# Kernel optimization log

Measured on AMD Instinct MI355X. Metric: run time of the kernel, lower is better.

## Reference

```python
import jax, jax.numpy as jnp
import numpy as np
import math

HIDDEN = 256
NUM_LAYERS = 3
NUM_TAU = 4
DT = 0.05
TAU_MIN, TAU_MAX = 0.01, 10.0
IN_SIZE = 128
OUT_SIZE = 64
B, S = 64, 2048


def setup_inputs() -> dict:
    key = jax.random.key(0)
    ks = jax.random.split(key, 16)
    H = HIDDEN
    def xavier(k, shape):
        fan_in, fan_out = shape[1], shape[0]
        lim = math.sqrt(6.0 / (fan_in + fan_out))
        return jax.random.uniform(k, shape, jnp.float32, -lim, lim)
    def ortho(k, n):
        a = jax.random.normal(k, (n, n), jnp.float32)
        q, r = jnp.linalg.qr(a)
        return q * jnp.sign(jnp.diag(r))[None, :]
    x = jax.random.normal(ks[0], (B, S, IN_SIZE), jnp.float32)
    # complexity_net: Linear(in,64) -> ReLU -> Linear(64,1) -> Sigmoid
    cw1 = xavier(ks[1], (64, IN_SIZE)); cb1 = jnp.zeros((64,), jnp.float32)
    cw2 = xavier(ks[2], (1, 64)); cb2 = jnp.zeros((1,), jnp.float32)
    # input projection
    pw = xavier(ks[3], (H, IN_SIZE)); pb = jnp.zeros((H,), jnp.float32)
    # per-layer recurrent params (stacked over layers)
    W_rec = jnp.stack([ortho(jax.random.fold_in(ks[4], i), H) for i in range(NUM_LAYERS)])
    W_in = jnp.stack([xavier(jax.random.fold_in(ks[5], i), (H, H)) for i in range(NUM_LAYERS)])
    bias = jnp.zeros((NUM_LAYERS, H), jnp.float32)
    tau_bands = jnp.tile(jnp.logspace(math.log10(TAU_MIN), math.log10(TAU_MAX), NUM_TAU, dtype=jnp.float32)[None, :], (NUM_LAYERS, 1))
    # tau_mixer: Linear(1, NUM_TAU) per layer -> weight [NUM_TAU,1] stored as [NUM_TAU]
    tmw = jax.random.uniform(ks[6], (NUM_LAYERS, NUM_TAU), jnp.float32, -1.0, 1.0)
    tmb = jax.random.uniform(ks[7], (NUM_LAYERS, NUM_TAU), jnp.float32, -1.0, 1.0)
    # output projection
    ow = xavier(ks[8], (OUT_SIZE, H)); ob = jnp.zeros((OUT_SIZE,), jnp.float32)
    return {"x": x, "cw1": cw1, "cb1": cb1, "cw2": cw2, "cb2": cb2,
            "pw": pw, "pb": pb, "W_rec": W_rec, "W_in": W_in, "bias": bias,
            "tau_bands": tau_bands, "tmw": tmw, "tmb": tmb, "ow": ow, "ob": ob}


def reference(x, cw1, cb1, cw2, cb2, pw, pb, W_rec, W_in, bias, tau_bands, tmw, tmb, ow, ob):
    # complexity net on time-mean of inputs -> [B, 1]
    comp = jax.nn.sigmoid(jax.nn.relu(x.mean(axis=1) @ cw1.T + cb1) @ cw2.T + cb2)
    h_seq = x @ pw.T + pb  # [B, S, H]
    hidden = jnp.zeros((x.shape[0], HIDDEN), x.dtype)
    for i in range(NUM_LAYERS):
        # tau_mixer: comp [B,1] * weight [NUM_TAU] -> logits [B, NUM_TAU]
        w = jax.nn.softmax(comp * tmw[i] + tmb[i], axis=-1)
        mixed_tau = jnp.sum(tau_bands[i] * w, axis=-1)          # [B]
        alpha = jnp.exp(-DT / mixed_tau)[:, None]               # [B,1] broadcast over H
        Wr, Wi, b = W_rec[i], W_in[i], bias[i]
        ext = h_seq @ Wi.T + b                                  # precompute input drive [B,S,H]
        def step(h, xt):
            act = jnp.tanh(h @ Wr.T + xt)
            h_new = alpha * h + (1.0 - alpha) * act
            return h_new, h_new
        hidden, outs = jax.lax.scan(step, hidden, ext.transpose(1, 0, 2))
        h_seq = outs.transpose(1, 0, 2)                         # [B,S,H]
    out = h_seq @ ow.T + ob                                     # [B,S,out]
    return out[:, -1]                                           # [B,out]
```

## Files before the change

### kernel.cpp

```cpp
#include <hip/hip_runtime.h>
#include <hip/hip_bf16.h>
#include <math.h>
#include <type_traits>

#define HIDDEN 256
#define SEQ 2048
#define BATCH 64
#define INSZ 128
#define OUTSZ 64
#define DTC 0.05f
#define CCH 32
#define CHS (SEQ / CCH)
#define TBLK (CHS / 32)

typedef _Float16 f16x8 __attribute__((ext_vector_type(8)));
typedef float f32x4 __attribute__((ext_vector_type(4)));

__global__ __launch_bounds__(1024) void prep_kernel(
    const float* __restrict__ x, const float* __restrict__ cw1, const float* __restrict__ cb1,
    const float* __restrict__ cw2, const float* __restrict__ cb2,
    const float* __restrict__ tau_b, const float* __restrict__ tmw, const float* __restrict__ tmb,
    float* __restrict__ alphas, float* __restrict__ h_carry)
{
    __shared__ float p_lds[8][128];
    __shared__ float xm[128];
    __shared__ float t1[64];
    int b = blockIdx.x;
    int tid = threadIdx.x;
    if (tid < 256) {
        h_carry[0 * 16384 + b * 256 + tid] = 0.f;
        h_carry[1 * 16384 + b * 256 + tid] = 0.f;
        h_carry[2 * 16384 + b * 256 + tid] = 0.f;
    }
    int c = tid & 127, sh = tid >> 7;
    const float* xb = x + (size_t)b * SEQ * INSZ;
    float s = 0.f;
    for (int t = sh * 256; t < (sh + 1) * 256; ++t) s += xb[(size_t)t * INSZ + c];
    p_lds[sh][c] = s;
    __syncthreads();
    if (tid < 128) {
        float m = 0.f;
        #pragma unroll
        for (int i = 0; i < 8; ++i) m += p_lds[i][tid];
        xm[tid] = m / (float)SEQ;
    }
    __syncthreads();
    if (tid < 64) {
        float acc = cb1[tid];
        for (int k = 0; k < 128; ++k) acc += xm[k] * cw1[tid * 128 + k];
        t1[tid] = fmaxf(acc, 0.f);
    }
    __syncthreads();
    if (tid == 0) {
        float acc = cb2[0];
        for (int k = 0; k < 64; ++k) acc += t1[k] * cw2[k];
        float comp = 1.f / (1.f + expf(-acc));
        for (int i = 0; i < 3; ++i) {
            float lg[4], mx = -1e30f;
            for (int j = 0; j < 4; ++j) { lg[j] = comp * tmw[i * 4 + j] + tmb[i * 4 + j]; mx = fmaxf(mx, lg[j]); }
            float den = 0.f;
            for (int j = 0; j < 4; ++j) { lg[j] = expf(lg[j] - mx); den += lg[j]; }
            float mt = 0.f;
            for (int j = 0; j < 4; ++j) mt += tau_b[i * 4 + j] * (lg[j] / den);
            alphas[i * 64 + b] = expf(-DTC / mt);
        }
    }
}

__global__ __launch_bounds__(128) void wf_kernel(
    const float* __restrict__ W_in0, const float* __restrict__ pw,
    const float* __restrict__ pb, const float* __restrict__ bias0,
    float* __restrict__ Wf, float* __restrict__ bf)
{
    __shared__ float wrow[256];
    int j = blockIdx.x, k = threadIdx.x;
    for (int m = k; m < 256; m += 128) wrow[m] = W_in0[j * 256 + m];
    __syncthreads();
    float s = 0.f;
    for (int m = 0; m < 256; ++m) s = fmaf(wrow[m], pw[m * 128 + k], s);
    Wf[j * 128 + k] = s;
    if (k == 0) {
        float sb = bias0[j];
        for (int m = 0; m < 256; ++m) sb = fmaf(wrow[m], pb[m], sb);
        bf[j] = sb;
    }
}

__device__ __forceinline__ unsigned pkrtz(float a, float b) {
    return __builtin_bit_cast(unsigned, __builtin_amdgcn_cvt_pkrtz(a, b));
}

__global__ __launch_bounds__(64) void wpack_kernel(
    const float* __restrict__ W, _Float16* __restrict__ P)
{
    int blk = blockIdx.x;
    int wave = blk >> 5, mt = (blk >> 3) & 3, kt = blk & 7;
    int lane = threadIdx.x;
    int row = wave * 64 + mt * 16 + (lane & 15);
    int kcol = kt * 32 + (lane >> 4) * 8;
    const float4* s = (const float4*)(W + (size_t)row * 256 + kcol);
    float4 a = s[0], b = s[1];
    uint4 u = { pkrtz(a.x, a.y), pkrtz(a.z, a.w), pkrtz(b.x, b.y), pkrtz(b.z, b.w) };
    *(uint4*)((char*)P + (size_t)blk * 1024 + lane * 16) = u;
}

__device__ __forceinline__ float fast_tanh(float x) {
    float ex = __expf(2.f * x);
    float r = __builtin_amdgcn_rcpf(ex + 1.f);
    return 1.f - 2.f * r;
}

__device__ __forceinline__ void barrier_lds_only() {
    asm volatile("s_waitcnt lgkmcnt(0)\n\ts_barrier" ::: "memory");
}

__global__ __launch_bounds__(256, 2) void gemm0_kernel(
    const float* __restrict__ Asrc,
    const float* __restrict__ W,
    const float* __restrict__ bias,
    float* __restrict__ C)
{
    constexpr int KD = 128, KT = 4, ROWB = 256;
    __shared__ alignas(16) char alds[32 * ROWB];
    const int tid = threadIdx.x;
    const int wave = tid >> 6, lane = tid & 63;
    const int bl = lane & 15, q = lane >> 4;
    const int m0 = blockIdx.x * 32;

    f16x8 bfrag[4][KT];
    float bv[4];
    #pragma unroll
    for (int nt = 0; nt < 4; ++nt) {
        int n = wave * 64 + nt * 16 + bl;
        const float* wr = W + (size_t)n * KD;
        #pragma unroll
        for (int kt = 0; kt < KT; ++kt) {
            const float4* wp = (const float4*)(wr + kt * 32 + q * 8);
            float4 u0 = wp[0], u1 = wp[1];
            uint4 u = { pkrtz(u0.x, u0.y), pkrtz(u0.z, u0.w),
                        pkrtz(u1.x, u1.y), pkrtz(u1.z, u1.w) };
            bfrag[nt][kt] = __builtin_bit_cast(f16x8, u);
        }
        bv[nt] = bias[n];
    }
    #pragma unroll
    for (int it = 0; it < 2; ++it) {
        int idx = tid + it * 256;
        int row = idx >> 4, chunk = idx & 15;
        const float4* sp = (const float4*)(Asrc + (size_t)(m0 + row) * KD + chunk * 8);
        float4 f0 = sp[0], f1 = sp[1];
        uint4 u = { pkrtz(f0.x, f0.y), pkrtz(f0.z, f0.w),
                    pkrtz(f1.x, f1.y), pkrtz(f1.z, f1.w) };
        *(uint4*)(alds + row * ROWB + ((chunk * 16) ^ ((row & 7) << 4))) = u;
    }
    __syncthreads();

    f32x4 acc[2][4];
    #pragma unroll
    for (int mt = 0; mt < 2; ++mt)
        #pragma unroll
        for (int nt = 0; nt < 4; ++nt) acc[mt][nt] = (f32x4){0.f, 0.f, 0.f, 0.f};
    #pragma unroll
    for (int kt = 0; kt < KT; ++kt) {
        int inner = kt * 64 + q * 16;
        f16x8 a0 = __builtin_bit_cast(f16x8,
            *(const uint4*)(alds + (0 * 16 + bl) * ROWB + (inner ^ ((bl & 7) << 4))));
        f16x8 a1 = __builtin_bit_cast(f16x8,
            *(const uint4*)(alds + (1 * 16 + bl) * ROWB + (inner ^ ((bl & 7) << 4))));
        #pragma unroll
        for (int nt = 0; nt < 4; ++nt) {
            acc[0][nt] = __builtin_amdgcn_mfma_f32_16x16x32_f16(a0, bfrag[nt][kt], acc[0][nt], 0, 0, 0);
            acc[1][nt] = __builtin_amdgcn_mfma_f32_16x16x32_f16(a1, bfrag[nt][kt], acc[1][nt], 0, 0, 0);
        }
    }
    #pragma unroll
    for (int mt = 0; mt < 2; ++mt)
        #pragma unroll
        for (int nt = 0; nt < 4; ++nt) {
            int col = wave * 64 + nt * 16 + bl;
            #pragma unroll
            for (int r = 0; r < 4; ++r)
                C[(size_t)(m0 + mt * 16 + q * 4 + r) * 256 + col] = acc[mt][nt][r] + bv[nt];
        }
}

__device__ __forceinline__ void scan_chunk(
    char* smem, float* buf, const _Float16* __restrict__ Wp,
    const float* __restrict__ alphas, float* __restrict__ h_carry,
    int b, int c, int write_all)
{
    _Float16 (*hlds)[256] = (_Float16 (*)[256])smem;
    const int tid = threadIdx.x;
    const int wave = tid >> 6, lane = tid & 63;
    const int bl = lane & 15, q = lane >> 4;
    const int mt_own = bl >> 2, r_own = bl & 3;
    const int m = wave * 64 + mt_own * 16 + q * 4 + r_own;

    f16x8 afrag[4][8];
    #pragma unroll
    for (int mt = 0; mt < 4; ++mt)
        #pragma unroll
        for (int kt = 0; kt < 8; ++kt)
            afrag[mt][kt] = __builtin_bit_cast(f16x8,
                *(const uint4*)((const char*)Wp + (size_t)(((wave * 4 + mt) * 8 + kt) * 64 + lane) * 16));

    const float alpha = alphas[b], onema = 1.f - alpha;
    float* bb = buf + (size_t)b * SEQ * HIDDEN;
    const int t0 = c * CHS, tend = t0 + CHS;

    float h_reg = h_carry[b * 256 + m];
    hlds[0][m] = (_Float16)h_reg;
    float e_cur = bb[(size_t)t0 * HIDDEN + m];
    float e_n1  = bb[(size_t)(t0 + 1) * HIDDEN + m];
    __syncthreads();

    auto step = [&](auto CB, int t) {
        constexpr int CUR = decltype(CB)::value;
        const char* rb = (const char*)&hlds[CUR][0];
        uint4 bq0 = *(const uint4*)(rb + q * 16);
        uint4 bq1 = *(const uint4*)(rb + 64 + q * 16);
        uint4 bq2 = *(const uint4*)(rb + 128 + q * 16);
        uint4 bq3 = *(const uint4*)(rb + 192 + q * 16);
        uint4 bq4 = *(const uint4*)(rb + 256 + q * 16);
        uint4 bq5 = *(const uint4*)(rb + 320 + q * 16);
        uint4 bq6 = *(const uint4*)(rb + 384 + q * 16);
        uint4 bq7 = *(const uint4*)(rb + 448 + q * 16);
        float e_n2 = 0.f;
        if (t + 2 < tend) e_n2 = bb[(size_t)(t + 2) * HIDDEN + m];

        f32x4 a0 = {0.f,0.f,0.f,0.f}, a1 = {0.f,0.f,0.f,0.f};
        f32x4 a2 = {0.f,0.f,0.f,0.f}, a3 = {0.f,0.f,0.f,0.f};
        #define MSTEP(BQ, KT) { f16x8 bf = __builtin_bit_cast(f16x8, BQ);                  \
            a0 = __builtin_amdgcn_mfma_f32_16x16x32_f16(afrag[0][KT], bf, a0, 0, 0, 0);    \
            a1 = __builtin_amdgcn_mfma_f32_16x16x32_f16(afrag[1][KT], bf, a1, 0, 0, 0);    \
            a2 = __builtin_amdgcn_mfma_f32_16x16x32_f16(afrag[2][KT], bf, a2, 0, 0, 0);    \
            a3 = __builtin_amdgcn_mfma_f32_16x16x32_f16(afrag[3][KT], bf, a3, 0, 0, 0); }
        MSTEP(bq0, 0) MSTEP(bq1, 1) MSTEP(bq2, 2) MSTEP(bq3, 3)
        MSTEP(bq4, 4) MSTEP(bq5, 5) MSTEP(bq6, 6) MSTEP(bq7, 7)
        #undef MSTEP

        f32x4 am = (mt_own == 0) ? a0 : (mt_own == 1) ? a1 : (mt_own == 2) ? a2 : a3;
        float s  = (r_own == 0) ? am[0] : (r_own == 1) ? am[1] : (r_own == 2) ? am[2] : am[3];

        float act = fast_tanh(s + e_cur);
        h_reg = alpha * h_reg + onema * act;
        hlds[CUR ^ 1][m] = (_Float16)h_reg;
        if (write_all)
            *((_Float16*)(bb + (size_t)t * HIDDEN) + m) = (_Float16)h_reg;
        barrier_lds_only();
        e_cur = e_n1;
        e_n1 = e_n2;
    };

    for (int t = t0; t < tend; t += 2) {
        step(std::integral_constant<int, 0>{}, t);
        step(std::integral_constant<int, 1>{}, t + 1);
    }
    h_carry[b * 256 + m] = h_reg;
}

__device__ __forceinline__ void gemm_chunk4(
    char* smem, float* buf, const _Float16* __restrict__ Wp,
    const float* __restrict__ bias, int gl, int c)
{
    constexpr int KT = 8, ROWB = 512;
    char* alds = smem;
    const int tid = threadIdx.x;
    const int wave = tid >> 6, lane = tid & 63;
    const int bl = lane & 15, q = lane >> 4;

    f16x8 bfrag[4][KT];
    float bv[4];
    #pragma unroll
    for (int nt = 0; nt < 4; ++nt) {
        #pragma unroll
        for (int kt = 0; kt < KT; ++kt)
            bfrag[nt][kt] = __builtin_bit_cast(f16x8,
                *(const uint4*)((const char*)Wp + (size_t)(((wave * 4 + nt) * 8 + kt) * 64 + lane) * 16));
        bv[nt] = bias[wave * 64 + nt * 16 + bl];
    }

    for (int u = 0; u < 2 * TBLK; ++u) {
        int b = 2 * gl + (u >> 1);
        int half = u & 1;
        size_t m0 = (size_t)b * SEQ + (size_t)c * CHS + (size_t)half * 32;

        __syncthreads();
        #pragma unroll
        for (int it = 0; it < 4; ++it) {
            int idx = tid + it * 256;
            int row = idx >> 5, chunk = idx & 31;
            uint4 uu = *(const uint4*)((const char*)buf + (m0 + row) * 1024 + chunk * 16);
            *(uint4*)(alds + row * ROWB + ((chunk * 16) ^ ((row & 7) << 4))) = uu;
        }
        __syncthreads();

        f32x4 acc[2][4];
        #pragma unroll
        for (int mt = 0; mt < 2; ++mt)
            #pragma unroll
            for (int nt = 0; nt < 4; ++nt) acc[mt][nt] = (f32x4){0.f, 0.f, 0.f, 0.f};
        #pragma unroll
        for (int kt = 0; kt < KT; ++kt) {
            int inner = kt * 64 + q * 16;
            f16x8 a0 = __builtin_bit_cast(f16x8,
                *(const uint4*)(alds + (0 * 16 + bl) * ROWB + (inner ^ ((bl & 7) << 4))));
            f16x8 a1 = __builtin_bit_cast(f16x8,
                *(const uint4*)(alds + (1 * 16 + bl) * ROWB + (inner ^ ((bl & 7) << 4))));
            #pragma unroll
            for (int nt = 0; nt < 4; ++nt) {
                acc[0][nt] = __builtin_amdgcn_mfma_f32_16x16x32_f16(a0, bfrag[nt][kt], acc[0][nt], 0, 0, 0);
                acc[1][nt] = __builtin_amdgcn_mfma_f32_16x16x32_f16(a1, bfrag[nt][kt], acc[1][nt], 0, 0, 0);
            }
        }
        #pragma unroll
        for (int mt = 0; mt < 2; ++mt)
            #pragma unroll
            for (int nt = 0; nt < 4; ++nt) {
                int col = wave * 64 + nt * 16 + bl;
                #pragma unroll
                for (int r = 0; r < 4; ++r)
                    buf[(m0 + mt * 16 + q * 4 + r) * 256 + col] = acc[mt][nt][r] + bv[nt];
            }
    }
}

__global__ __launch_bounds__(256, 1) void stage_kernel(
    int stage, float* buf,
    const _Float16* __restrict__ wpk,
    const float* __restrict__ bias,  const float* __restrict__ alphas,
    float* __restrict__ h_carry)
{
    __shared__ alignas(16) char smem[16384];
    int blk = blockIdx.x;
    if (blk < 192) {
        int layer = blk >> 6;
        int c = stage - 2 * layer;
        if (c < 0 || c >= CCH) return;
        scan_chunk(smem, buf, wpk + (size_t)layer * 65536, alphas + layer * 64,
                   h_carry + (size_t)layer * 16384, blk & 63, c, layer < 2);
    } else {
        int g = blk - 192;
        int which = g >> 5;
        int gl = g & 31;
        int c = stage - 1 - 2 * which;
        if (c < 0 || c >= CCH) return;
        gemm_chunk4(smem, buf, wpk + (size_t)(3 + which) * 65536, bias + (which + 1) * 256, gl, c);
    }
}

__global__ __launch_bounds__(256) void outproj_kernel(
    const float* __restrict__ h_carry, const float* __restrict__ ow, const float* __restrict__ ob,
    float* __restrict__ out)
{
    __shared__ float h_l[256];
    __shared__ float p_lds[4][64];
    int b = blockIdx.x;
    int tid = threadIdx.x;
    h_l[tid] = h_carry[b * 256 + tid];
    __syncthreads();
    int o = tid & 63, qq = tid >> 6;
    float s = 0.f;
    const float4* wp = (const float4*)(ow + o * 256 + qq * 64);
    const float4* hp = (const float4*)(h_l + qq * 64);
    #pragma unroll
    for (int m = 0; m < 16; ++m) {
        float4 wv = wp[m]; float4 hv = hp[m];
        s = fmaf(wv.x, hv.x, s); s = fmaf(wv.y, hv.y, s);
        s = fmaf(wv.z, hv.z, s); s = fmaf(wv.w, hv.w, s);
    }
    p_lds[qq][o] = s;
    __syncthreads();
    if (tid < 64)
        out[b * 64 + tid] = p_lds[0][tid] + p_lds[1][tid] + p_lds[2][tid] + p_lds[3][tid] + ob[tid];
}

extern "C" void kernel_launch(void* const* d_in, const int* in_sizes, int n_in,
                              void* d_out, int out_size, void* d_ws, size_t ws_size,
                              hipStream_t stream)
{
    const float* x     = (const float*)d_in[0];
    const float* cw1   = (const float*)d_in[1];
    const float* cb1   = (const float*)d_in[2];
    const float* cw2   = (const float*)d_in[3];
    const float* cb2   = (const float*)d_in[4];
    const float* pw    = (const float*)d_in[5];
    const float* pb    = (const float*)d_in[6];
    const float* W_rec = (const float*)d_in[7];
    const float* W_in  = (const float*)d_in[8];
    const float* bias  = (const float*)d_in[9];
    const float* tau_b = (const float*)d_in[10];
    const float* tmw   = (const float*)d_in[11];
    const float* tmb   = (const float*)d_in[12];
    const float* ow    = (const float*)d_in[13];
    const float* ob    = (const float*)d_in[14];
    float* out = (float*)d_out;

    char* ws = (char*)d_ws;
    float*     alphas  = (float*)ws;
    float*     h_carry = (float*)(ws + 1024);
    float*     bf      = (float*)(ws + 197632);
    float*     Wf      = (float*)(ws + 198656);
    _Float16*  wpk     = (_Float16*)(ws + 329728);
    float*     buf     = (float*)(ws + 1048576);

    const int MROWS = BATCH * SEQ;
    const int NGBLK = 256;

    prep_kernel<<<64, 1024, 0, stream>>>(x, cw1, cb1, cw2, cb2, tau_b, tmw, tmb, alphas, h_carry);
    wf_kernel<<<256, 128, 0, stream>>>(W_in, pw, pb, bias, Wf, bf);

    wpack_kernel<<<128, 64, 0, stream>>>(W_rec,                wpk);
    wpack_kernel<<<128, 64, 0, stream>>>(W_rec + 65536,        wpk + 65536);
    wpack_kernel<<<128, 64, 0, stream>>>(W_rec + 131072,       wpk + 2 * 65536);
    wpack_kernel<<<128, 64, 0, stream>>>(W_in + 65536,         wpk + 3 * 65536);
    wpack_kernel<<<128, 64, 0, stream>>>(W_in + 131072,        wpk + 4 * 65536);

    gemm0_kernel<<<MROWS / 32, 256, 0, stream>>>(x, Wf, bf, buf);

    for (int s = 0; s < CCH + 4; ++s)
        stage_kernel<<<NGBLK, 256, 0, stream>>>(s, buf, wpk, bias, alphas, h_carry);

    outproj_kernel<<<64, 256, 0, stream>>>(h_carry + 2 * 16384, ow, ob, out);
}
```

Before: 1.504 ms.

## Fuse per-stage launches into one cooperative persistent kernel with grid sync

Replaces the loop of 36 stage_kernel launches with a single cooperative persistent kernel that loops over stages and uses grid.sync between them. Scan blocks keep the hidden state in registers across chunks instead of reloading it from h_carry, and each block loads its weight fragments into registers once instead of every stage. The change targets per-launch overhead and repeated weight/state reloads, at the cost of a grid-wide barrier per stage and the requirement that all 256 blocks be co-resident.

After: 3.112 ms. 107% more time.

```diff
diff --git a/kernel.cpp b/kernel.cpp
--- a/kernel.cpp
+++ b/kernel.cpp
@@ -1,7 +1,10 @@
 #include <hip/hip_runtime.h>
 #include <hip/hip_bf16.h>
+#include <hip/hip_cooperative_groups.h>
 #include <math.h>
 #include <type_traits>
+
+namespace cg = cooperative_groups;
 
 #define HIDDEN 256
 #define SEQ 2048
@@ -20,18 +23,13 @@
     const float* __restrict__ x, const float* __restrict__ cw1, const float* __restrict__ cb1,
     const float* __restrict__ cw2, const float* __restrict__ cb2,
     const float* __restrict__ tau_b, const float* __restrict__ tmw, const float* __restrict__ tmb,
-    float* __restrict__ alphas, float* __restrict__ h_carry)
+    float* __restrict__ alphas)
 {
     __shared__ float p_lds[8][128];
     __shared__ float xm[128];
     __shared__ float t1[64];
     int b = blockIdx.x;
     int tid = threadIdx.x;
-    if (tid < 256) {
-        h_carry[0 * 16384 + b * 256 + tid] = 0.f;
-        h_carry[1 * 16384 + b * 256 + tid] = 0.f;
-        h_carry[2 * 16384 + b * 256 + tid] = 0.f;
-    }
     int c = tid & 127, sh = tid >> 7;
     const float* xb = x + (size_t)b * SEQ * INSZ;
     float s = 0.f;
@@ -115,10 +113,8 @@
 }
 
 __global__ __launch_bounds__(256, 2) void gemm0_kernel(
-    const float* __restrict__ Asrc,
-    const float* __restrict__ W,
-    const float* __restrict__ bias,
-    float* __restrict__ C)
+    const float* __restrict__ Asrc, const float* __restrict__ W,
+    const float* __restrict__ bias, float* __restrict__ C)
 {
     constexpr int KD = 128, KT = 4, ROWB = 256;
     __shared__ alignas(16) char alds[32 * ROWB];
@@ -184,168 +180,167 @@
         }
 }
 
-__device__ __forceinline__ void scan_chunk(
-    char* smem, float* buf, const _Float16* __restrict__ Wp,
-    const float* __restrict__ alphas, float* __restrict__ h_carry,
-    int b, int c, int write_all)
-{
-    _Float16 (*hlds)[256] = (_Float16 (*)[256])smem;
+__global__ __launch_bounds__(256, 1) void persist_kernel(
+    float* __restrict__ buf,
+    const _Float16* __restrict__ wpk,
+    const float* __restrict__ bias,
+    const float* __restrict__ alphas,
+    float* __restrict__ h_carry)
+{
+    cg::grid_group grid = cg::this_grid();
+    __shared__ alignas(16) char smem[16384];
+    const int blk = blockIdx.x;
     const int tid = threadIdx.x;
-    const int wave = tid >> 6, lane = tid & 63;
-    const int bl = lane & 15, q = lane >> 4;
-    const int mt_own = bl >> 2, r_own = bl & 3;
-    const int m = wave * 64 + mt_own * 16 + q * 4 + r_own;
-
-    f16x8 afrag[4][8];
-    #pragma unroll
-    for (int mt = 0; mt < 4; ++mt)
-        #pragma unroll
-        for (int kt = 0; kt < 8; ++kt)
-            afrag[mt][kt] = __builtin_bit_cast(f16x8,
-                *(const uint4*)((const char*)Wp + (size_t)(((wave * 4 + mt) * 8 + kt) * 64 + lane) * 16));
-
-    const float alpha = alphas[b], onema = 1.f - alpha;
-    float* bb = buf + (size_t)b * SEQ * HIDDEN;
-    const int t0 = c * CHS, tend = t0 + CHS;
-
-    float h_reg = h_carry[b * 256 + m];
-    hlds[0][m] = (_Float16)h_reg;
-    float e_cur = bb[(size_t)t0 * HIDDEN + m];
-    float e_n1  = bb[(size_t)(t0 + 1) * HIDDEN + m];
-    __syncthreads();
-
-    auto step = [&](auto CB, int t) {
-        constexpr int CUR = decltype(CB)::value;
-        const char* rb = (const char*)&hlds[CUR][0];
-        uint4 bq0 = *(const uint4*)(rb + q * 16);
-        uint4 bq1 = *(const uint4*)(rb + 64 + q * 16);
-        uint4 bq2 = *(const uint4*)(rb + 128 + q * 16);
-        uint4 bq3 = *(const uint4*)(rb + 192 + q * 16);
-        uint4 bq4 = *(const uint4*)(rb + 256 + q * 16);
-        uint4 bq5 = *(const uint4*)(rb + 320 + q * 16);
-        uint4 bq6 = *(const uint4*)(rb + 384 + q * 16);
-        uint4 bq7 = *(const uint4*)(rb + 448 + q * 16);
-        float e_n2 = 0.f;
-        if (t + 2 < tend) e_n2 = bb[(size_t)(t + 2) * HIDDEN + m];
-
-        f32x4 a0 = {0.f,0.f,0.f,0.f}, a1 = {0.f,0.f,0.f,0.f};
-        f32x4 a2 = {0.f,0.f,0.f,0.f}, a3 = {0.f,0.f,0.f,0.f};
-        #define MSTEP(BQ, KT) { f16x8 bf = __builtin_bit_cast(f16x8, BQ);                  \
-            a0 = __builtin_amdgcn_mfma_f32_16x16x32_f16(afrag[0][KT], bf, a0, 0, 0, 0);    \
-            a1 = __builtin_amdgcn_mfma_f32_16x16x32_f16(afrag[1][KT], bf, a1, 0, 0, 0);    \
-            a2 = __builtin_amdgcn_mfma_f32_16x16x32_f16(afrag[2][KT], bf, a2, 0, 0, 0);    \
-            a3 = __builtin_amdgcn_mfma_f32_16x16x32_f16(afrag[3][KT], bf, a3, 0, 0, 0); }
-        MSTEP(bq0, 0) MSTEP(bq1, 1) MSTEP(bq2, 2) MSTEP(bq3, 3)
-        MSTEP(bq4, 4) MSTEP(bq5, 5) MSTEP(bq6, 6) MSTEP(bq7, 7)
-        #undef MSTEP
-
-        f32x4 am = (mt_own == 0) ? a0 : (mt_own == 1) ? a1 : (mt_own == 2) ? a2 : a3;
-        float s  = (r_own == 0) ? am[0] : (r_own == 1) ? am[1] : (r_own == 2) ? am[2] : am[3];
-
-        float act = fast_tanh(s + e_cur);
-        h_reg = alpha * h_reg + onema * act;
-        hlds[CUR ^ 1][m] = (_Float16)h_reg;
-        if (write_all)
-            *((_Float16*)(bb + (size_t)t * HIDDEN) + m) = (_Float16)h_reg;
-        barrier_lds_only();
-        e_cur = e_n1;
-        e_n1 = e_n2;
-    };
-
-    for (int t = t0; t < tend; t += 2) {
-        step(std::integral_constant<int, 0>{}, t);
-        step(std::integral_constant<int, 1>{}, t + 1);
-    }
-    h_carry[b * 256 + m] = h_reg;
-}
-
-__device__ __forceinline__ void gemm_chunk4(
-    char* smem, float* buf, const _Float16* __restrict__ Wp,
-    const float* __restrict__ bias, int gl, int c)
-{
-    constexpr int KT = 8, ROWB = 512;
-    char* alds = smem;
-    const int tid = threadIdx.x;
-    const int wave = tid >> 6, lane = tid & 63;
-    const int bl = lane & 15, q = lane >> 4;
-
-    f16x8 bfrag[4][KT];
-    float bv[4];
-    #pragma unroll
-    for (int nt = 0; nt < 4; ++nt) {
-        #pragma unroll
-        for (int kt = 0; kt < KT; ++kt)
-            bfrag[nt][kt] = __builtin_bit_cast(f16x8,
-                *(const uint4*)((const char*)Wp + (size_t)(((wave * 4 + nt) * 8 + kt) * 64 + lane) * 16));
-        bv[nt] = bias[wave * 64 + nt * 16 + bl];
-    }
-
-    for (int u = 0; u < 2 * TBLK; ++u) {
-        int b = 2 * gl + (u >> 1);
-        int half = u & 1;
-        size_t m0 = (size_t)b * SEQ + (size_t)c * CHS + (size_t)half * 32;
-
-        __syncthreads();
-        #pragma unroll
-        for (int it = 0; it < 4; ++it) {
-            int idx = tid + it * 256;
-            int row = idx >> 5, chunk = idx & 31;
-            uint4 uu = *(const uint4*)((const char*)buf + (m0 + row) * 1024 + chunk * 16);
-            *(uint4*)(alds + row * ROWB + ((chunk * 16) ^ ((row & 7) << 4))) = uu;
-        }
-        __syncthreads();
-
-        f32x4 acc[2][4];
-        #pragma unroll
-        for (int mt = 0; mt < 2; ++mt)
+
+    if (blk < 192) {
+        const int layer = blk >> 6, b = blk & 63;
+        const int wave = tid >> 6, lane = tid & 63;
+        const int bl = lane & 15, q = lane >> 4;
+        const int mt_own = bl >> 2, r_own = bl & 3;
+        const int m = wave * 64 + mt_own * 16 + q * 4 + r_own;
+        const _Float16* Wp = wpk + (size_t)layer * 65536;
+        _Float16 (*hlds)[256] = (_Float16 (*)[256])smem;
+
+        f16x8 afrag[4][8];
+        #pragma unroll
+        for (int mt = 0; mt < 4; ++mt)
             #pragma unroll
-            for (int nt = 0; nt < 4; ++nt) acc[mt][nt] = (f32x4){0.f, 0.f, 0.f, 0.f};
-        #pragma unroll
-        for (int kt = 0; kt < KT; ++kt) {
-            int inner = kt * 64 + q * 16;
-            f16x8 a0 = __builtin_bit_cast(f16x8,
-                *(const uint4*)(alds + (0 * 16 + bl) * ROWB + (inner ^ ((bl & 7) << 4))));
-            f16x8 a1 = __builtin_bit_cast(f16x8,
-                *(const uint4*)(alds + (1 * 16 + bl) * ROWB + (inner ^ ((bl & 7) << 4))));
+            for (int kt = 0; kt < 8; ++kt)
+                afrag[mt][kt] = __builtin_bit_cast(f16x8,
+                    *(const uint4*)((const char*)Wp + (size_t)(((wave * 4 + mt) * 8 + kt) * 64 + lane) * 16));
+
+        const float alpha = alphas[layer * 64 + b], onema = 1.f - alpha;
+        float* bb = buf + (size_t)b * SEQ * HIDDEN;
+        const int write_all = (layer < 2);
+        float h_reg = 0.f;
+
+        for (int s = 0; s < CCH + 4; ++s) {
+            int c = s - 2 * layer;
+            if (c >= 0 && c < CCH) {
+                const int t0 = c * CHS, tend = t0 + CHS;
+                hlds[0][m] = (_Float16)h_reg;
+                float e_cur = bb[(size_t)t0 * HIDDEN + m];
+                float e_n1  = bb[(size_t)(t0 + 1) * HIDDEN + m];
+                __syncthreads();
+
+                auto step = [&](auto CB, int t) {
+                    constexpr int CUR = decltype(CB)::value;
+                    const char* rb = (const char*)&hlds[CUR][0];
+                    uint4 bq0 = *(const uint4*)(rb + q * 16);
+                    uint4 bq1 = *(const uint4*)(rb + 64 + q * 16);
+                    uint4 bq2 = *(const uint4*)(rb + 128 + q * 16);
+                    uint4 bq3 = *(const uint4*)(rb + 192 + q * 16);
+                    uint4 bq4 = *(const uint4*)(rb + 256 + q * 16);
+                    uint4 bq5 = *(const uint4*)(rb + 320 + q * 16);
+                    uint4 bq6 = *(const uint4*)(rb + 384 + q * 16);
+                    uint4 bq7 = *(const uint4*)(rb + 448 + q * 16);
+                    float e_n2 = 0.f;
+                    if (t + 2 < tend) e_n2 = bb[(size_t)(t + 2) * HIDDEN + m];
+
+                    f32x4 a0 = {0.f,0.f,0.f,0.f}, a1 = {0.f,0.f,0.f,0.f};
+                    f32x4 a2 = {0.f,0.f,0.f,0.f}, a3 = {0.f,0.f,0.f,0.f};
+                    #define MSTEP(BQ, KT) { f16x8 bf = __builtin_bit_cast(f16x8, BQ);                  \
+                        a0 = __builtin_amdgcn_mfma_f32_16x16x32_f16(afrag[0][KT], bf, a0, 0, 0, 0);    \
+                        a1 = __builtin_amdgcn_mfma_f32_16x16x32_f16(afrag[1][KT], bf, a1, 0, 0, 0);    \
+                        a2 = __builtin_amdgcn_mfma_f32_16x16x32_f16(afrag[2][KT], bf, a2, 0, 0, 0);    \
+                        a3 = __builtin_amdgcn_mfma_f32_16x16x32_f16(afrag[3][KT], bf, a3, 0, 0, 0); }
+                    MSTEP(bq0, 0) MSTEP(bq1, 1) MSTEP(bq2, 2) MSTEP(bq3, 3)
+                    MSTEP(bq4, 4) MSTEP(bq5, 5) MSTEP(bq6, 6) MSTEP(bq7, 7)
+                    #undef MSTEP
+
+                    f32x4 am = (mt_own == 0) ? a0 : (mt_own == 1) ? a1 : (mt_own == 2) ? a2 : a3;
+                    float sv = (r_own == 0) ? am[0] : (r_own == 1) ? am[1] : (r_own == 2) ? am[2] : am[3];
+
+                    float act = fast_tanh(sv + e_cur);
+                    h_reg = alpha * h_reg + onema * act;
+                    hlds[CUR ^ 1][m] = (_Float16)h_reg;
+                    if (write_all)
+                        *((_Float16*)(bb + (size_t)t * HIDDEN) + m) = (_Float16)h_reg;
+                    barrier_lds_only();
+                    e_cur = e_n1;
+                    e_n1 = e_n2;
+                };
+
+                for (int t = t0; t < tend; t += 2) {
+                    step(std::integral_constant<int, 0>{}, t);
+                    step(std::integral_constant<int, 1>{}, t + 1);
+                }
+            }
+            __threadfence();
+            grid.sync();
+        }
+        if (layer == 2) h_carry[2 * 16384 + b * 256 + m] = h_reg;
+    } else {
+        constexpr int KT = 8, ROWB = 512;
+        char* alds = smem;
+        const int g = blk - 192;
+        const int which = g >> 5, gl = g & 31;
+        const int wave = tid >> 6, lane = tid & 63;
+        const int bl = lane & 15, q = lane >> 4;
+        const _Float16* Wp = wpk + (size_t)(3 + which) * 65536;
+        const float* bias_l = bias + (which + 1) * 256;
+
+        f16x8 bfrag[4][KT];
+        float bv[4];
+        #pragma unroll
+        for (int nt = 0; nt < 4; ++nt) {
             #pragma unroll
-            for (int nt = 0; nt < 4; ++nt) {
-                acc[0][nt] = __builtin_amdgcn_mfma_f32_16x16x32_f16(a0, bfrag[nt][kt], acc[0][nt], 0, 0, 0);
-                acc[1][nt] = __builtin_amdgcn_mfma_f32_16x16x32_f16(a1, bfrag[nt][kt], acc[1][nt], 0, 0, 0);
+            for (int kt = 0; kt < KT; ++kt)
+                bfrag[nt][kt] = __builtin_bit_cast(f16x8,
+                    *(const uint4*)((const char*)Wp + (size_t)(((wave * 4 + nt) * 8 + kt) * 64 + lane) * 16));
+            bv[nt] = bias_l[wave * 64 + nt * 16 + bl];
+        }
+
+        for (int s = 0; s < CCH + 4; ++s) {
+            int c = s - 1 - 2 * which;
+            if (c >= 0 && c < CCH) {
+                for (int u = 0; u < 2 * TBLK; ++u) {
+                    int b = 2 * gl + (u >> 1);
+                    int half = u & 1;
+                    size_t m0 = (size_t)b * SEQ + (size_t)c * CHS + (size_t)half * 32;
+
+                    __syncthreads();
+                    #pragma unroll
+                    for (int it = 0; it < 4; ++it) {
+                        int idx = tid + it * 256;
+                        int row = idx >> 5, chunk = idx & 31;
+                        uint4 uu = *(const uint4*)((const char*)buf + (m0 + row) * 1024 + chunk * 16);
+                        *(uint4*)(alds + row * ROWB + ((chunk * 16) ^ ((row & 7) << 4))) = uu;
+                    }
+                    __syncthreads();
+
+                    f32x4 acc[2][4];
+                    #pragma unroll
+                    for (int mt = 0; mt < 2; ++mt)
+                        #pragma unroll
+                        for (int nt = 0; nt < 4; ++nt) acc[mt][nt] = (f32x4){0.f, 0.f, 0.f, 0.f};
+                    #pragma unroll
+                    for (int kt = 0; kt < KT; ++kt) {
+                        int inner = kt * 64 + q * 16;
+                        f16x8 a0 = __builtin_bit_cast(f16x8,
+                            *(const uint4*)(alds + (0 * 16 + bl) * ROWB + (inner ^ ((bl & 7) << 4))));
+                        f16x8 a1 = __builtin_bit_cast(f16x8,
+                            *(const uint4*)(alds + (1 * 16 + bl) * ROWB + (inner ^ ((bl & 7) << 4))));
+                        #pragma unroll
+                        for (int nt = 0; nt < 4; ++nt) {
+                            acc[0][nt] = __builtin_amdgcn_mfma_f32_16x16x32_f16(a0, bfrag[nt][kt], acc[0][nt], 0, 0, 0);
+                            acc[1][nt] = __builtin_amdgcn_mfma_f32_16x16x32_f16(a1, bfrag[nt][kt], acc[1][nt], 0, 0, 0);
+                        }
+                    }
+                    #pragma unroll
+                    for (int mt = 0; mt < 2; ++mt)
+                        #pragma unroll
+                        for (int nt = 0; nt < 4; ++nt) {
+                            int col = wave * 64 + nt * 16 + bl;
+                            #pragma unroll
+                            for (int r = 0; r < 4; ++r)
+                                buf[(m0 + mt * 16 + q * 4 + r) * 256 + col] = acc[mt][nt][r] + bv[nt];
+                        }
+                }
             }
-        }
-        #pragma unroll
-        for (int mt = 0; mt < 2; ++mt)
-            #pragma unroll
-            for (int nt = 0; nt < 4; ++nt) {
-                int col = wave * 64 + nt * 16 + bl;
-                #pragma unroll
-                for (int r = 0; r < 4; ++r)
-                    buf[(m0 + mt * 16 + q * 4 + r) * 256 + col] = acc[mt][nt][r] + bv[nt];
-            }
-    }
-}
-
-__global__ __launch_bounds__(256, 1) void stage_kernel(
-    int stage, float* buf,
-    const _Float16* __restrict__ wpk,
-    const float* __restrict__ bias,  const float* __restrict__ alphas,
-    float* __restrict__ h_carry)
-{
-    __shared__ alignas(16) char smem[16384];
-    int blk = blockIdx.x;
-    if (blk < 192) {
-        int layer = blk >> 6;
-        int c = stage - 2 * layer;
-        if (c < 0 || c >= CCH) return;
-        scan_chunk(smem, buf, wpk + (size_t)layer * 65536, alphas + layer * 64,
-                   h_carry + (size_t)layer * 16384, blk & 63, c, layer < 2);
-    } else {
-        int g = blk - 192;
-        int which = g >> 5;
-        int gl = g & 31;
-        int c = stage - 1 - 2 * which;
-        if (c < 0 || c >= CCH) return;
-        gemm_chunk4(smem, buf, wpk + (size_t)(3 + which) * 65536, bias + (which + 1) * 256, gl, c);
+            __threadfence();
+            grid.sync();
+        }
     }
 }
 
@@ -405,21 +400,28 @@
     float*     buf     = (float*)(ws + 1048576);
 
     const int MROWS = BATCH * SEQ;
-    const int NGBLK = 256;
-
-    prep_kernel<<<64, 1024, 0, stream>>>(x, cw1, cb1, cw2, cb2, tau_b, tmw, tmb, alphas, h_carry);
+
+    prep_kernel<<<64, 1024, 0, stream>>>(x, cw1, cb1, cw2, cb2, tau_b, tmw, tmb, alphas);
     wf_kernel<<<256, 128, 0, stream>>>(W_in, pw, pb, bias, Wf, bf);
 
-    wpack_kernel<<<128, 64, 0, stream>>>(W_rec,                wpk);
-    wpack_kernel<<<128, 64, 0, stream>>>(W_rec + 65536,        wpk + 65536);
-    wpack_kernel<<<128, 64, 0, stream>>>(W_rec + 131072,       wpk + 2 * 65536);
-    wpack_kernel<<<128, 64, 0, stream>>>(W_in + 65536,         wpk + 3 * 65536);
-    wpack_kernel<<<128, 64, 0, stream>>>(W_in + 131072,        wpk + 4 * 65536);
+    wpack_kernel<<<128, 64, 0, stream>>>(W_rec,          wpk);
+    wpack_kernel<<<128, 64, 0, stream>>>(W_rec + 65536,  wpk + 65536);
+    wpack_kernel<<<128, 64, 0, stream>>>(W_rec + 131072, wpk + 2 * 65536);
+    wpack_kernel<<<128, 64, 0, stream>>>(W_in + 65536,   wpk + 3 * 65536);
+    wpack_kernel<<<128, 64, 0, stream>>>(W_in + 131072,  wpk + 4 * 65536);
 
     gemm0_kernel<<<MROWS / 32, 256, 0, stream>>>(x, Wf, bf, buf);
 
-    for (int s = 0; s < CCH + 4; ++s)
-        stage_kernel<<<NGBLK, 256, 0, stream>>>(s, buf, wpk, bias, alphas, h_carry);
+    {
+        float* buf_p = buf;
+        const _Float16* wpk_p = wpk;
+        const float* bias_p = bias;
+        const float* alphas_p = alphas;
+        float* hc_p = h_carry;
+        void* kargs[] = { &buf_p, &wpk_p, &bias_p, &alphas_p, &hc_p };
+        hipLaunchCooperativeKernel((const void*)persist_kernel, dim3(256), dim3(256),
+                                   kargs, 0, stream);
+    }
 
     outproj_kernel<<<64, 256, 0, stream>>>(h_carry + 2 * 16384, ow, ob, out);
 }
```

## Fold input projection GEMM into the staged wavefront pipeline

Applied to the files above, without the earlier changes.

The standalone full-sequence gemm0 kernel is removed. Its work is split into per-chunk tasks handled by 64 extra blocks in the stage kernel, so the layer-0 input projection for chunk c runs alongside the scans and later-layer GEMMs of earlier chunks. The stage offsets shift by one and the pipeline gains two stages, which adds launches and lengthens the dependency chain by one stage. In exchange, the upfront GEMM no longer has to finish before the first scan can start.

New measurement: 1.449 ms. 3.7% less time.

```diff
diff --git a/kernel.cpp b/kernel.cpp
--- a/kernel.cpp
+++ b/kernel.cpp
@@ -112,76 +112,6 @@
 
 __device__ __forceinline__ void barrier_lds_only() {
     asm volatile("s_waitcnt lgkmcnt(0)\n\ts_barrier" ::: "memory");
-}
-
-__global__ __launch_bounds__(256, 2) void gemm0_kernel(
-    const float* __restrict__ Asrc,
-    const float* __restrict__ W,
-    const float* __restrict__ bias,
-    float* __restrict__ C)
-{
-    constexpr int KD = 128, KT = 4, ROWB = 256;
-    __shared__ alignas(16) char alds[32 * ROWB];
-    const int tid = threadIdx.x;
-    const int wave = tid >> 6, lane = tid & 63;
-    const int bl = lane & 15, q = lane >> 4;
-    const int m0 = blockIdx.x * 32;
-
-    f16x8 bfrag[4][KT];
-    float bv[4];
-    #pragma unroll
-    for (int nt = 0; nt < 4; ++nt) {
-        int n = wave * 64 + nt * 16 + bl;
-        const float* wr = W + (size_t)n * KD;
-        #pragma unroll
-        for (int kt = 0; kt < KT; ++kt) {
-            const float4* wp = (const float4*)(wr + kt * 32 + q * 8);
-            float4 u0 = wp[0], u1 = wp[1];
-            uint4 u = { pkrtz(u0.x, u0.y), pkrtz(u0.z, u0.w),
-                        pkrtz(u1.x, u1.y), pkrtz(u1.z, u1.w) };
-            bfrag[nt][kt] = __builtin_bit_cast(f16x8, u);
-        }
-        bv[nt] = bias[n];
-    }
-    #pragma unroll
-    for (int it = 0; it < 2; ++it) {
-        int idx = tid + it * 256;
-        int row = idx >> 4, chunk = idx & 15;
-        const float4* sp = (const float4*)(Asrc + (size_t)(m0 + row) * KD + chunk * 8);
-        float4 f0 = sp[0], f1 = sp[1];
-        uint4 u = { pkrtz(f0.x, f0.y), pkrtz(f0.z, f0.w),
-                    pkrtz(f1.x, f1.y), pkrtz(f1.z, f1.w) };
-        *(uint4*)(alds + row * ROWB + ((chunk * 16) ^ ((row & 7) << 4))) = u;
-    }
-    __syncthreads();
-
-    f32x4 acc[2][4];
-    #pragma unroll
-    for (int mt = 0; mt < 2; ++mt)
-        #pragma unroll
-        for (int nt = 0; nt < 4; ++nt) acc[mt][nt] = (f32x4){0.f, 0.f, 0.f, 0.f};
-    #pragma unroll
-    for (int kt = 0; kt < KT; ++kt) {
-        int inner = kt * 64 + q * 16;
-        f16x8 a0 = __builtin_bit_cast(f16x8,
-            *(const uint4*)(alds + (0 * 16 + bl) * ROWB + (inner ^ ((bl & 7) << 4))));
-        f16x8 a1 = __builtin_bit_cast(f16x8,
-            *(const uint4*)(alds + (1 * 16 + bl) * ROWB + (inner ^ ((bl & 7) << 4))));
-        #pragma unroll
-        for (int nt = 0; nt < 4; ++nt) {
-            acc[0][nt] = __builtin_amdgcn_mfma_f32_16x16x32_f16(a0, bfrag[nt][kt], acc[0][nt], 0, 0, 0);
-            acc[1][nt] = __builtin_amdgcn_mfma_f32_16x16x32_f16(a1, bfrag[nt][kt], acc[1][nt], 0, 0, 0);
-        }
-    }
-    #pragma unroll
-    for (int mt = 0; mt < 2; ++mt)
-        #pragma unroll
-        for (int nt = 0; nt < 4; ++nt) {
-            int col = wave * 64 + nt * 16 + bl;
-            #pragma unroll
-            for (int r = 0; r < 4; ++r)
-                C[(size_t)(m0 + mt * 16 + q * 4 + r) * 256 + col] = acc[mt][nt][r] + bv[nt];
-        }
 }
 
 __device__ __forceinline__ void scan_chunk(
@@ -230,19 +160,19 @@
 
         f32x4 a0 = {0.f,0.f,0.f,0.f}, a1 = {0.f,0.f,0.f,0.f};
         f32x4 a2 = {0.f,0.f,0.f,0.f}, a3 = {0.f,0.f,0.f,0.f};
-        #define MSTEP(BQ, KT) { f16x8 bf = __builtin_bit_cast(f16x8, BQ);                  \
-            a0 = __builtin_amdgcn_mfma_f32_16x16x32_f16(afrag[0][KT], bf, a0, 0, 0, 0);    \
-            a1 = __builtin_amdgcn_mfma_f32_16x16x32_f16(afrag[1][KT], bf, a1, 0, 0, 0);    \
-            a2 = __builtin_amdgcn_mfma_f32_16x16x32_f16(afrag[2][KT], bf, a2, 0, 0, 0);    \
-            a3 = __builtin_amdgcn_mfma_f32_16x16x32_f16(afrag[3][KT], bf, a3, 0, 0, 0); }
+        #define MSTEP(BQ, KT) { f16x8 bf_ = __builtin_bit_cast(f16x8, BQ);                 \
+            a0 = __builtin_amdgcn_mfma_f32_16x16x32_f16(afrag[0][KT], bf_, a0, 0, 0, 0);   \
+            a1 = __builtin_amdgcn_mfma_f32_16x16x32_f16(afrag[1][KT], bf_, a1, 0, 0, 0);   \
+            a2 = __builtin_amdgcn_mfma_f32_16x16x32_f16(afrag[2][KT], bf_, a2, 0, 0, 0);   \
+            a3 = __builtin_amdgcn_mfma_f32_16x16x32_f16(afrag[3][KT], bf_, a3, 0, 0, 0); }
         MSTEP(bq0, 0) MSTEP(bq1, 1) MSTEP(bq2, 2) MSTEP(bq3, 3)
         MSTEP(bq4, 4) MSTEP(bq5, 5) MSTEP(bq6, 6) MSTEP(bq7, 7)
         #undef MSTEP
 
         f32x4 am = (mt_own == 0) ? a0 : (mt_own == 1) ? a1 : (mt_own == 2) ? a2 : a3;
-        float s  = (r_own == 0) ? am[0] : (r_own == 1) ? am[1] : (r_own == 2) ? am[2] : am[3];
-
-        float act = fast_tanh(s + e_cur);
+        float sv = (r_own == 0) ? am[0] : (r_own == 1) ? am[1] : (r_own == 2) ? am[2] : am[3];
+
+        float act = fast_tanh(sv + e_cur);
         h_reg = alpha * h_reg + onema * act;
         hlds[CUR ^ 1][m] = (_Float16)h_reg;
         if (write_all)
@@ -325,9 +255,84 @@
     }
 }
 
+__device__ __forceinline__ void gemm0_chunk(
+    char* smem, const float* __restrict__ x, const float* __restrict__ Wf,
+    const float* __restrict__ bf, float* __restrict__ buf, int gl, int c)
+{
+    constexpr int KD = 128, KT = 4, ROWB = 256;
+    char* alds = smem;
+    const int tid = threadIdx.x;
+    const int wave = tid >> 6, lane = tid & 63;
+    const int bl = lane & 15, q = lane >> 4;
+
+    f16x8 bfrag[4][KT];
+    float bv[4];
+    #pragma unroll
+    for (int nt = 0; nt < 4; ++nt) {
+        int n = wave * 64 + nt * 16 + bl;
+        const float* wr = Wf + (size_t)n * KD;
+        #pragma unroll
+        for (int kt = 0; kt < KT; ++kt) {
+            const float4* wp = (const float4*)(wr + kt * 32 + q * 8);
+            float4 u0 = wp[0], u1 = wp[1];
+            uint4 u = { pkrtz(u0.x, u0.y), pkrtz(u0.z, u0.w),
+                        pkrtz(u1.x, u1.y), pkrtz(u1.z, u1.w) };
+            bfrag[nt][kt] = __builtin_bit_cast(f16x8, u);
+        }
+        bv[nt] = bf[n];
+    }
+
+    for (int half = 0; half < 2; ++half) {
+        size_t m0 = (size_t)gl * SEQ + (size_t)c * CHS + (size_t)half * 32;
+        const float* Asrc = x + m0 * KD;
+
+        __syncthreads();
+        #pragma unroll
+        for (int it = 0; it < 2; ++it) {
+            int idx = tid + it * 256;
+            int row = idx >> 4, chunk = idx & 15;
+            const float4* sp = (const float4*)(Asrc + (size_t)row * KD + chunk * 8);
+            float4 f0 = sp[0], f1 = sp[1];
+            uint4 u = { pkrtz(f0.x, f0.y), pkrtz(f0.z, f0.w),
+                        pkrtz(f1.x, f1.y), pkrtz(f1.z, f1.w) };
+            *(uint4*)(alds + row * ROWB + ((chunk * 16) ^ ((row & 7) << 4))) = u;
+        }
+        __syncthreads();
+
+        f32x4 acc[2][4];
+        #pragma unroll
+        for (int mt = 0; mt < 2; ++mt)
+            #pragma unroll
+            for (int nt = 0; nt < 4; ++nt) acc[mt][nt] = (f32x4){0.f, 0.f, 0.f, 0.f};
+        #pragma unroll
+        for (int kt = 0; kt < KT; ++kt) {
+            int inner = kt * 64 + q * 16;
+            f16x8 a0 = __builtin_bit_cast(f16x8,
+                *(const uint4*)(alds + (0 * 16 + bl) * ROWB + (inner ^ ((bl & 7) << 4))));
+            f16x8 a1 = __builtin_bit_cast(f16x8,
+                *(const uint4*)(alds + (1 * 16 + bl) * ROWB + (inner ^ ((bl & 7) << 4))));
+            #pragma unroll
+            for (int nt = 0; nt < 4; ++nt) {
+                acc[0][nt] = __builtin_amdgcn_mfma_f32_16x16x32_f16(a0, bfrag[nt][kt], acc[0][nt], 0, 0, 0);
+                acc[1][nt] = __builtin_amdgcn_mfma_f32_16x16x32_f16(a1, bfrag[nt][kt], acc[1][nt], 0, 0, 0);
+            }
+        }
+        #pragma unroll
+        for (int mt = 0; mt < 2; ++mt)
+            #pragma unroll
+            for (int nt = 0; nt < 4; ++nt) {
+                int col = wave * 64 + nt * 16 + bl;
+                #pragma unroll
+                for (int r = 0; r < 4; ++r)
+                    buf[(m0 + mt * 16 + q * 4 + r) * 256 + col] = acc[mt][nt][r] + bv[nt];
+            }
+    }
+}
+
 __global__ __launch_bounds__(256, 1) void stage_kernel(
-    int stage, float* buf,
+    int stage, float* buf, const float* __restrict__ x,
     const _Float16* __restrict__ wpk,
+    const float* __restrict__ Wf, const float* __restrict__ bf,
     const float* __restrict__ bias,  const float* __restrict__ alphas,
     float* __restrict__ h_carry)
 {
@@ -335,17 +340,22 @@
     int blk = blockIdx.x;
     if (blk < 192) {
         int layer = blk >> 6;
-        int c = stage - 2 * layer;
+        int c = stage - 1 - 2 * layer;
         if (c < 0 || c >= CCH) return;
         scan_chunk(smem, buf, wpk + (size_t)layer * 65536, alphas + layer * 64,
                    h_carry + (size_t)layer * 16384, blk & 63, c, layer < 2);
-    } else {
+    } else if (blk < 256) {
         int g = blk - 192;
         int which = g >> 5;
         int gl = g & 31;
-        int c = stage - 1 - 2 * which;
+        int c = stage - 2 - 2 * which;
         if (c < 0 || c >= CCH) return;
         gemm_chunk4(smem, buf, wpk + (size_t)(3 + which) * 65536, bias + (which + 1) * 256, gl, c);
+    } else {
+        int gl = blk - 256;
+        int c = stage;
+        if (c >= CCH) return;
+        gemm0_chunk(smem, x, Wf, bf, buf, gl, c);
     }
 }
 
@@ -404,22 +414,17 @@
     _Float16*  wpk     = (_Float16*)(ws + 329728);
     float*     buf     = (float*)(ws + 1048576);
 
-    const int MROWS = BATCH * SEQ;
-    const int NGBLK = 256;
-
     prep_kernel<<<64, 1024, 0, stream>>>(x, cw1, cb1, cw2, cb2, tau_b, tmw, tmb, alphas, h_carry);
     wf_kernel<<<256, 128, 0, stream>>>(W_in, pw, pb, bias, Wf, bf);
 
-    wpack_kernel<<<128, 64, 0, stream>>>(W_rec,                wpk);
-    wpack_kernel<<<128, 64, 0, stream>>>(W_rec + 65536,        wpk + 65536);
-    wpack_kernel<<<128, 64, 0, stream>>>(W_rec + 131072,       wpk + 2 * 65536);
-    wpack_kernel<<<128, 64, 0, stream>>>(W_in + 65536,         wpk + 3 * 65536);
-    wpack_kernel<<<128, 64, 0, stream>>>(W_in + 131072,        wpk + 4 * 65536);
-
-    gemm0_kernel<<<MROWS / 32, 256, 0, stream>>>(x, Wf, bf, buf);
-
-    for (int s = 0; s < CCH + 4; ++s)
-        stage_kernel<<<NGBLK, 256, 0, stream>>>(s, buf, wpk, bias, alphas, h_carry);
+    wpack_kernel<<<128, 64, 0, stream>>>(W_rec,          wpk);
+    wpack_kernel<<<128, 64, 0, stream>>>(W_rec + 65536,  wpk + 65536);
+    wpack_kernel<<<128, 64, 0, stream>>>(W_rec + 131072, wpk + 2 * 65536);
+    wpack_kernel<<<128, 64, 0, stream>>>(W_in + 65536,   wpk + 3 * 65536);
+    wpack_kernel<<<128, 64, 0, stream>>>(W_in + 131072,  wpk + 4 * 65536);
+
+    for (int s = 0; s < CCH + 6; ++s)
+        stage_kernel<<<320, 256, 0, stream>>>(s, buf, x, wpk, Wf, bf, bias, alphas, h_carry);
 
     outproj_kernel<<<64, 256, 0, stream>>>(h_carry + 2 * 16384, ow, ob, out);
 }
```
